# Kernel tuning notes

Measured on AMD Instinct MI355X. Metric: run time of the kernel, lower is better.

## Reference

```python
import jax, jax.numpy as jnp
import numpy as np

T, B, H = 1024, 4096, 4  # time steps, students, BKT params (l,f,g,s)


def setup_inputs() -> dict:
    key = jax.random.key(0)
    ks = jax.random.split(key, 6)
    # binary correctness sequences, like the original BKT data
    x = (jax.random.uniform(ks[0], (T, B, 1)) < 0.5).astype(jnp.float32)
    y = (jax.random.uniform(ks[1], (T, B, 1)) < 0.5).astype(jnp.float32)
    s = 1.0 / np.sqrt(H)  # torch nn.RNN default init: U(-1/sqrt(H), 1/sqrt(H))
    W_ih = jax.random.uniform(ks[2], (H, 1), minval=-s, maxval=s, dtype=jnp.float32)
    W_hh = jax.random.uniform(ks[3], (H, H), minval=-s, maxval=s, dtype=jnp.float32)
    b_ih = jax.random.uniform(ks[4], (H,), minval=-s, maxval=s, dtype=jnp.float32)
    b_hh = jax.random.uniform(ks[5], (H,), minval=-s, maxval=s, dtype=jnp.float32)
    prior = jnp.array([0.1], dtype=jnp.float32)
    return {"x": x, "y": y, "prior": prior, "W_ih": W_ih, "W_hh": W_hh,
            "b_ih": b_ih, "b_hh": b_hh}


def _bce(p, y):
    # torch BCELoss clamps log terms at -100
    logp = jnp.maximum(jnp.log(p), -100.0)
    log1mp = jnp.maximum(jnp.log(1.0 - p), -100.0)
    return -(y * logp + (1.0 - y) * log1mp).mean()


def _forward(x, y, prior, W_ih, W_hh, b_ih, b_hh):
    Bn = x.shape[1]
    Hn = W_hh.shape[0]

    # --- Elman RNN (tanh), seq-first, h0 = 0 ---
    def rnn_step(h, x_t):  # x_t: [B,1], h: [B,H]
        h = jnp.tanh(x_t @ W_ih.T + b_ih + h @ W_hh.T + b_hh)
        return h, h

    h0 = jnp.zeros((Bn, Hn), dtype=x.dtype)
    _, output = jax.lax.scan(rnn_step, h0, x)  # [T,B,H]
    params = (output + 1.0) / 2.0  # map tanh output into (0,1)

    # --- sequential nonlinear BKT latent recurrence ---
    latent0 = jnp.broadcast_to(jax.nn.sigmoid(prior), (Bn, 1)).astype(x.dtype)

    def bkt_step(latent, inp):
        p_t, y_t = inp  # p_t: [B,H], y_t: [B,1]
        l, f, g, s = p_t[:, 0:1], p_t[:, 1:2], p_t[:, 2:3], p_t[:, 3:4]
        correct = latent * (1 - s) + (1 - latent) * g
        k_t1 = latent * (1 - s) / (latent * (1 - s) + (1 - latent) * g)
        k_t0 = latent * s / (latent * s + (1 - latent) * (1 - g))
        m_t = k_t1 * correct + k_t0 * (1 - correct)
        next_latent = m_t * (1 - f) + (1 - m_t) * l
        return next_latent, (correct, next_latent, _bce(correct, y_t))

    _, (corrects, latents, losses) = jax.lax.scan(bkt_step, latent0, (params, y))
    loss = losses.mean()  # sum of per-step BCE / T
    return corrects, latents, loss


def reference(x, y, prior, W_ih, W_hh, b_ih, b_hh):
    return _forward(x, y, prior, W_ih, W_hh, b_ih, b_hh)
```

## Files before the change

### kernel.cpp

```cpp
#include <hip/hip_runtime.h>

#define TT 1024
#define BB 4096
#define CHUNK 64
#define WH 64
#define NCH (TT / CHUNK)
#define NB  (NCH * BB)

#define WS_A   1024
#define WS_B   (WS_A + NB)
#define WS_H   (WS_B + NB)
#define WS_XW  (WS_H + 4 * NB)

typedef float v2f __attribute__((ext_vector_type(2)));

struct StepC {
    v2f base01, base23, sw01, sw23;
    v2f c0_01, c0_23, c1_01, c1_23, c2_01, c2_23, c3_01, c3_23;
};

__device__ __forceinline__ StepC make_consts(const float* W_ih, const float* W_hh,
                                             const float* b_ih, const float* b_hh) {
    const float S = 2.8853900817779268f;
    float basev[4], swv[4], vv[4][4];
    #pragma unroll
    for (int jj = 0; jj < 4; ++jj) {
        float rowsum = W_hh[jj*4+0] + W_hh[jj*4+1] + W_hh[jj*4+2] + W_hh[jj*4+3];
        basev[jj] = S * (b_ih[jj] + b_hh[jj] + rowsum);
        swv[jj]   = S * W_ih[jj];
        #pragma unroll
        for (int kk = 0; kk < 4; ++kk) vv[jj][kk] = -2.f * S * W_hh[jj*4+kk];
    }
    StepC K;
    K.base01 = {basev[0], basev[1]}; K.base23 = {basev[2], basev[3]};
    K.sw01   = {swv[0],   swv[1]};   K.sw23   = {swv[2],   swv[3]};
    K.c0_01 = {vv[0][0], vv[1][0]};  K.c0_23 = {vv[2][0], vv[3][0]};
    K.c1_01 = {vv[0][1], vv[1][1]};  K.c1_23 = {vv[2][1], vv[3][1]};
    K.c2_01 = {vv[0][2], vv[1][2]};  K.c2_23 = {vv[2][2], vv[3][2]};
    K.c3_01 = {vv[0][3], vv[1][3]};  K.c3_23 = {vv[2][3], vv[3][3]};
    return K;
}

__device__ __forceinline__ void rnn_step(const StepC& K, float xf,
                                         float& r0, float& r1, float& r2, float& r3) {
    v2f xv  = {xf, xf};
    v2f r0b = {r0, r0}, r1b = {r1, r1}, r2b = {r2, r2}, r3b = {r3, r3};
    v2f z01 = __builtin_elementwise_fma(xv, K.sw01, K.base01);
    v2f z23 = __builtin_elementwise_fma(xv, K.sw23, K.base23);
    z01 = __builtin_elementwise_fma(r0b, K.c0_01, z01);
    z23 = __builtin_elementwise_fma(r0b, K.c0_23, z23);
    z01 = __builtin_elementwise_fma(r1b, K.c1_01, z01);
    z23 = __builtin_elementwise_fma(r1b, K.c1_23, z23);
    z01 = __builtin_elementwise_fma(r2b, K.c2_01, z01);
    z23 = __builtin_elementwise_fma(r2b, K.c2_23, z23);
    z01 = __builtin_elementwise_fma(r3b, K.c3_01, z01);
    z23 = __builtin_elementwise_fma(r3b, K.c3_23, z23);
    r0 = __builtin_amdgcn_rcpf(__builtin_amdgcn_exp2f(z01.x) + 1.0f);
    r1 = __builtin_amdgcn_rcpf(__builtin_amdgcn_exp2f(z01.y) + 1.0f);
    r2 = __builtin_amdgcn_rcpf(__builtin_amdgcn_exp2f(z23.x) + 1.0f);
    r3 = __builtin_amdgcn_rcpf(__builtin_amdgcn_exp2f(z23.y) + 1.0f);
}

__launch_bounds__(64, 1)
__global__ void bkt_pass1(const float* __restrict__ x,
                          const float* __restrict__ W_ih, const float* __restrict__ W_hh,
                          const float* __restrict__ b_ih, const float* __restrict__ b_hh,
                          float* __restrict__ ws)
{
    const int lane = threadIdx.x;
    const int c  = blockIdx.x >> 6;
    const int eg = blockIdx.x & 63;
    const int e  = eg * 64 + lane;
    const int t0 = c * CHUNK;
    const int t_start = (c == 0) ? 0 : (t0 - WH);
    const float* xp = x + (size_t)t_start * BB + e;

    float bufA[32], bufB[32];
    auto issueA = [&](int wd) {
        const float* p = xp + (size_t)wd * 32 * BB;
        #pragma unroll
        for (int i = 0; i < 32; ++i) bufA[i] = p[(size_t)i * BB];
    };
    auto issueB = [&](int wd) {
        const float* p = xp + (size_t)wd * 32 * BB;
        #pragma unroll
        for (int i = 0; i < 32; ++i) bufB[i] = p[(size_t)i * BB];
    };
    auto packA = [&]() -> unsigned {
        unsigned m = 0;
        #pragma unroll
        for (int i = 0; i < 32; ++i) if (bufA[i] != 0.0f) m |= (1u << i);
        return m;
    };
    auto packB = [&]() -> unsigned {
        unsigned m = 0;
        #pragma unroll
        for (int i = 0; i < 32; ++i) if (bufB[i] != 0.0f) m |= (1u << i);
        return m;
    };

    const StepC K = make_consts(W_ih, W_hh, b_ih, b_hh);
    float r0 = 0.5f, r1 = 0.5f, r2 = 0.5f, r3 = 0.5f;

    auto run32_warm = [&](unsigned m) {
        #pragma unroll 8
        for (int i = 0; i < 32; ++i)
            rnn_step(K, (float)((m >> i) & 1u), r0, r1, r2, r3);
    };

    float A = 1.0f, Bacc = 0.0f;
    auto run32_acc = [&](unsigned m) {
        #pragma unroll 8
        for (int i = 0; i < 32; ++i) {
            rnn_step(K, (float)((m >> i) & 1u), r0, r1, r2, r3);
            float a = (r0 + r1) - 1.0f;
            Bacc = fmaf(a, Bacc, 1.0f - r0);
            A *= a;
        }
    };

    float s0, s1, s2, s3;
    unsigned mo0, mo1;

    if (c == 0) {
        issueA(0); issueB(1);
        s0 = s1 = s2 = s3 = 0.5f;
        mo0 = packA();
        run32_acc(mo0);
        mo1 = packB();
        run32_acc(mo1);
    } else {
        issueA(0); issueB(1);
        unsigned mw0 = packA();
        issueA(2);
        run32_warm(mw0);
        unsigned mw1 = packB();
        issueB(3);
        run32_warm(mw1);
        s0 = r0; s1 = r1; s2 = r2; s3 = r3;
        mo0 = packA();
        run32_acc(mo0);
        mo1 = packB();
        run32_acc(mo1);
    }

    const int idx = c * BB + e;
    ws[WS_A + idx] = A;
    ws[WS_B + idx] = Bacc;
    ws[WS_H + 0 * NB + idx] = s0;
    ws[WS_H + 1 * NB + idx] = s1;
    ws[WS_H + 2 * NB + idx] = s2;
    ws[WS_H + 3 * NB + idx] = s3;
    unsigned* wsu = (unsigned*)ws;
    wsu[WS_XW + 0 * NB + idx] = mo0;
    wsu[WS_XW + 1 * NB + idx] = mo1;
}

__launch_bounds__(64, 1)
__global__ void bkt_pass2(const float* __restrict__ y, const float* __restrict__ prior,
                          const float* __restrict__ W_ih, const float* __restrict__ W_hh,
                          const float* __restrict__ b_ih, const float* __restrict__ b_hh,
                          float* __restrict__ out, float* __restrict__ ws)
{
    const int lane = threadIdx.x;
    const int c  = blockIdx.x >> 6;
    const int eg = blockIdx.x & 63;
    const int e  = eg * 64 + lane;
    const int t0 = c * CHUNK;
    const int idx = c * BB + e;

    float Av[NCH - 1], Bv[NCH - 1];
    #pragma unroll
    for (int cc = 0; cc < NCH - 1; ++cc) {
        Av[cc] = ws[WS_A + cc * BB + e];
        Bv[cc] = ws[WS_B + cc * BB + e];
    }
    float r0 = ws[WS_H + 0 * NB + idx];
    float r1 = ws[WS_H + 1 * NB + idx];
    float r2 = ws[WS_H + 2 * NB + idx];
    float r3 = ws[WS_H + 3 * NB + idx];
    const unsigned* wsu = (const unsigned*)ws;
    unsigned mo0 = wsu[WS_XW + 0 * NB + idx];
    unsigned mo1 = wsu[WS_XW + 1 * NB + idx];

    const float* ypb = y + (size_t)t0 * BB + e;
    float yA[32], yB[32];
    #pragma unroll
    for (int i = 0; i < 32; ++i) yA[i] = ypb[(size_t)i * BB];
    #pragma unroll
    for (int i = 0; i < 32; ++i) yB[i] = ypb[(size_t)(i + 32) * BB];

    const StepC K = make_consts(W_ih, W_hh, b_ih, b_hh);

    float lat = 1.0f / (1.0f + __builtin_amdgcn_exp2f(-1.4426950408889634f * prior[0]));
    #pragma unroll
    for (int cc = 0; cc < NCH - 1; ++cc)
        lat = (cc < c) ? fmaf(Av[cc], lat, Bv[cc]) : lat;

    unsigned yw0 = 0, yw1 = 0;
    #pragma unroll
    for (int i = 0; i < 32; ++i) {
        if (yA[i] != 0.0f) yw0 |= (1u << i);
        if (yB[i] != 0.0f) yw1 |= (1u << i);
    }

    float* cO = out + (size_t)t0 * BB + e;
    float* lO = cO + (size_t)TT * BB;
    float lossAcc = 0.0f;

    auto outblock = [&](unsigned mw, unsigned yw, int tb) {
        float prod = 1.0f;
        #pragma unroll 8
        for (int i = 0; i < 32; ++i) {
            rnn_step(K, (float)((mw >> i) & 1u), r0, r1, r2, r3);
            float corr = fmaf(lat, (r2 + r3) - 1.0f, 1.0f - r2);
            float nl   = fmaf(lat, (r0 + r1) - 1.0f, 1.0f - r0);
            const size_t off = (size_t)(tb + i) * BB;
            cO[off] = corr;
            lO[off] = nl;
            float lp = ((yw >> i) & 1u) ? corr : (1.0f - corr);
            prod *= lp;
            if ((i & 7) == 7) {
                lossAcc += __builtin_amdgcn_logf(prod) * 0.6931471805599453f;
                prod = 1.0f;
            }
            lat = nl;
        }
    };
    outblock(mo0, yw0, 0);
    outblock(mo1, yw1, 32);

    #pragma unroll
    for (int o = 32; o >= 1; o >>= 1) lossAcc += __shfl_xor(lossAcc, o, 64);
    if (lane == 0) ws[blockIdx.x] = lossAcc;
}

__global__ void reduce_k(const float* __restrict__ part, float* __restrict__ loss) {
    float acc = 0.f;
    for (int i = threadIdx.x; i < 1024; i += 256) acc += part[i];
    #pragma unroll
    for (int o = 32; o >= 1; o >>= 1) acc += __shfl_xor(acc, o, 64);
    __shared__ float w[4];
    if ((threadIdx.x & 63) == 0) w[threadIdx.x >> 6] = acc;
    __syncthreads();
    if (threadIdx.x == 0) {
        float t = w[0] + w[1] + w[2] + w[3];
        *loss = t * (-1.0f / ((float)TT * (float)BB));
    }
}

extern "C" void kernel_launch(void* const* d_in, const int* in_sizes, int n_in,
                              void* d_out, int out_size, void* d_ws, size_t ws_size,
                              hipStream_t stream) {
    const float* x    = (const float*)d_in[0];
    const float* y    = (const float*)d_in[1];
    const float* pr   = (const float*)d_in[2];
    const float* W_ih = (const float*)d_in[3];
    const float* W_hh = (const float*)d_in[4];
    const float* b_ih = (const float*)d_in[5];
    const float* b_hh = (const float*)d_in[6];
    float* out = (float*)d_out;
    float* ws  = (float*)d_ws;

    bkt_pass1<<<NCH * 64, 64, 0, stream>>>(x, W_ih, W_hh, b_ih, b_hh, ws);
    bkt_pass2<<<NCH * 64, 64, 0, stream>>>(y, pr, W_ih, W_hh, b_ih, b_hh, out, ws);
    reduce_k<<<1, 256, 0, stream>>>(ws, out + 2 * (size_t)TT * BB);
}
```

Before: 115.7 us.

## Fuse both BKT passes and loss reduction into one cooperative kernel with grid sync

Merges the two passes into a single cooperative kernel. The RNN hidden state and x bitmasks stay in registers across a grid-wide sync, so they are no longer written to and reread from workspace. The y loads are issued during the accumulation phase to overlap with compute. The separate reduce kernel is replaced by an atomic loss accumulation, with the last-arriving block writing the final loss. This removes two launches and workspace round-trips, but adds grid-sync cost, requires all 1024 blocks to be co-resident, and makes the loss sum order nondeterministic.

```diff
diff --git a/kernel.cpp b/kernel.cpp
--- a/kernel.cpp
+++ b/kernel.cpp
@@ -1,4 +1,7 @@
 #include <hip/hip_runtime.h>
+#include <hip/hip_cooperative_groups.h>
+
+namespace cg = cooperative_groups;
 
 #define TT 1024
 #define BB 4096
@@ -7,10 +10,10 @@
 #define NCH (TT / CHUNK)
 #define NB  (NCH * BB)
 
-#define WS_A   1024
-#define WS_B   (WS_A + NB)
-#define WS_H   (WS_B + NB)
-#define WS_XW  (WS_H + 4 * NB)
+#define WS_LOSS 0
+#define WS_CNT  1
+#define WS_A    64
+#define WS_B    (WS_A + NB)
 
 typedef float v2f __attribute__((ext_vector_type(2)));
 
@@ -62,102 +65,8 @@
 }
 
 __launch_bounds__(64, 1)
-__global__ void bkt_pass1(const float* __restrict__ x,
-                          const float* __restrict__ W_ih, const float* __restrict__ W_hh,
-                          const float* __restrict__ b_ih, const float* __restrict__ b_hh,
-                          float* __restrict__ ws)
-{
-    const int lane = threadIdx.x;
-    const int c  = blockIdx.x >> 6;
-    const int eg = blockIdx.x & 63;
-    const int e  = eg * 64 + lane;
-    const int t0 = c * CHUNK;
-    const int t_start = (c == 0) ? 0 : (t0 - WH);
-    const float* xp = x + (size_t)t_start * BB + e;
-
-    float bufA[32], bufB[32];
-    auto issueA = [&](int wd) {
-        const float* p = xp + (size_t)wd * 32 * BB;
-        #pragma unroll
-        for (int i = 0; i < 32; ++i) bufA[i] = p[(size_t)i * BB];
-    };
-    auto issueB = [&](int wd) {
-        const float* p = xp + (size_t)wd * 32 * BB;
-        #pragma unroll
-        for (int i = 0; i < 32; ++i) bufB[i] = p[(size_t)i * BB];
-    };
-    auto packA = [&]() -> unsigned {
-        unsigned m = 0;
-        #pragma unroll
-        for (int i = 0; i < 32; ++i) if (bufA[i] != 0.0f) m |= (1u << i);
-        return m;
-    };
-    auto packB = [&]() -> unsigned {
-        unsigned m = 0;
-        #pragma unroll
-        for (int i = 0; i < 32; ++i) if (bufB[i] != 0.0f) m |= (1u << i);
-        return m;
-    };
-
-    const StepC K = make_consts(W_ih, W_hh, b_ih, b_hh);
-    float r0 = 0.5f, r1 = 0.5f, r2 = 0.5f, r3 = 0.5f;
-
-    auto run32_warm = [&](unsigned m) {
-        #pragma unroll 8
-        for (int i = 0; i < 32; ++i)
-            rnn_step(K, (float)((m >> i) & 1u), r0, r1, r2, r3);
-    };
-
-    float A = 1.0f, Bacc = 0.0f;
-    auto run32_acc = [&](unsigned m) {
-        #pragma unroll 8
-        for (int i = 0; i < 32; ++i) {
-            rnn_step(K, (float)((m >> i) & 1u), r0, r1, r2, r3);
-            float a = (r0 + r1) - 1.0f;
-            Bacc = fmaf(a, Bacc, 1.0f - r0);
-            A *= a;
-        }
-    };
-
-    float s0, s1, s2, s3;
-    unsigned mo0, mo1;
-
-    if (c == 0) {
-        issueA(0); issueB(1);
-        s0 = s1 = s2 = s3 = 0.5f;
-        mo0 = packA();
-        run32_acc(mo0);
-        mo1 = packB();
-        run32_acc(mo1);
-    } else {
-        issueA(0); issueB(1);
-        unsigned mw0 = packA();
-        issueA(2);
-        run32_warm(mw0);
-        unsigned mw1 = packB();
-        issueB(3);
-        run32_warm(mw1);
-        s0 = r0; s1 = r1; s2 = r2; s3 = r3;
-        mo0 = packA();
-        run32_acc(mo0);
-        mo1 = packB();
-        run32_acc(mo1);
-    }
-
-    const int idx = c * BB + e;
-    ws[WS_A + idx] = A;
-    ws[WS_B + idx] = Bacc;
-    ws[WS_H + 0 * NB + idx] = s0;
-    ws[WS_H + 1 * NB + idx] = s1;
-    ws[WS_H + 2 * NB + idx] = s2;
-    ws[WS_H + 3 * NB + idx] = s3;
-    unsigned* wsu = (unsigned*)ws;
-    wsu[WS_XW + 0 * NB + idx] = mo0;
-    wsu[WS_XW + 1 * NB + idx] = mo1;
-}
-
-__launch_bounds__(64, 1)
-__global__ void bkt_pass2(const float* __restrict__ y, const float* __restrict__ prior,
+__global__ void bkt_fused(const float* __restrict__ x, const float* __restrict__ y,
+                          const float* __restrict__ prior,
                           const float* __restrict__ W_ih, const float* __restrict__ W_hh,
                           const float* __restrict__ b_ih, const float* __restrict__ b_hh,
                           float* __restrict__ out, float* __restrict__ ws)
@@ -167,7 +76,94 @@
     const int eg = blockIdx.x & 63;
     const int e  = eg * 64 + lane;
     const int t0 = c * CHUNK;
+    const int t_start = (c == 0) ? 0 : (t0 - WH);
+    const float* xp  = x + (size_t)t_start * BB + e;
+    const float* ypb = y + (size_t)t0 * BB + e;
+
+    if (blockIdx.x == 0 && lane == 0) {
+        ws[WS_LOSS] = 0.0f;
+        ((unsigned*)ws)[WS_CNT] = 0u;
+    }
+
+    float bufA[32], bufB[32];
+    auto issueA = [&](const float* p) {
+        #pragma unroll
+        for (int i = 0; i < 32; ++i) bufA[i] = p[(size_t)i * BB];
+    };
+    auto issueB = [&](const float* p) {
+        #pragma unroll
+        for (int i = 0; i < 32; ++i) bufB[i] = p[(size_t)i * BB];
+    };
+    auto packA = [&]() -> unsigned {
+        unsigned m = 0;
+        #pragma unroll
+        for (int i = 0; i < 32; ++i) if (bufA[i] != 0.0f) m |= (1u << i);
+        return m;
+    };
+    auto packB = [&]() -> unsigned {
+        unsigned m = 0;
+        #pragma unroll
+        for (int i = 0; i < 32; ++i) if (bufB[i] != 0.0f) m |= (1u << i);
+        return m;
+    };
+
+    issueA(xp); issueB(xp + (size_t)32 * BB);
+    const float pr0 = prior[0];
+    const StepC K = make_consts(W_ih, W_hh, b_ih, b_hh);
+
+    float r0 = 0.5f, r1 = 0.5f, r2 = 0.5f, r3 = 0.5f;
+    float A = 1.0f, Bacc = 0.0f;
+
+    auto run32_warm = [&](unsigned m) {
+        #pragma unroll 8
+        for (int i = 0; i < 32; ++i)
+            rnn_step(K, (float)((m >> i) & 1u), r0, r1, r2, r3);
+    };
+    auto run32_acc = [&](unsigned m) {
+        #pragma unroll 8
+        for (int i = 0; i < 32; ++i) {
+            rnn_step(K, (float)((m >> i) & 1u), r0, r1, r2, r3);
+            float a = (r0 + r1) - 1.0f;
+            Bacc = fmaf(a, Bacc, 1.0f - r0);
+            A *= a;
+        }
+    };
+
+    float s0, s1, s2, s3;
+    unsigned mo0, mo1, yw0, yw1;
+
+    if (c == 0) {
+        s0 = s1 = s2 = s3 = 0.5f;
+        mo0 = packA();
+        issueA(ypb);
+        run32_acc(mo0);
+        mo1 = packB();
+        issueB(ypb + (size_t)32 * BB);
+        run32_acc(mo1);
+        yw0 = packA(); yw1 = packB();
+    } else {
+        unsigned mw0 = packA();
+        issueA(xp + (size_t)64 * BB);
+        run32_warm(mw0);
+        unsigned mw1 = packB();
+        issueB(xp + (size_t)96 * BB);
+        run32_warm(mw1);
+        s0 = r0; s1 = r1; s2 = r2; s3 = r3;
+        mo0 = packA();
+        issueA(ypb);
+        run32_acc(mo0);
+        mo1 = packB();
+        issueB(ypb + (size_t)32 * BB);
+        run32_acc(mo1);
+        yw0 = packA(); yw1 = packB();
+    }
+
     const int idx = c * BB + e;
+    ws[WS_A + idx] = A;
+    ws[WS_B + idx] = Bacc;
+
+    __threadfence();
+    cg::this_grid().sync();
 
     float Av[NCH - 1], Bv[NCH - 1];
     #pragma unroll
@@ -175,35 +171,12 @@
         Av[cc] = ws[WS_A + cc * BB + e];
         Bv[cc] = ws[WS_B + cc * BB + e];
     }
-    float r0 = ws[WS_H + 0 * NB + idx];
-    float r1 = ws[WS_H + 1 * NB + idx];
-    float r2 = ws[WS_H + 2 * NB + idx];
-    float r3 = ws[WS_H + 3 * NB + idx];
-    const unsigned* wsu = (const unsigned*)ws;
-    unsigned mo0 = wsu[WS_XW + 0 * NB + idx];
-    unsigned mo1 = wsu[WS_XW + 1 * NB + idx];
-
-    const float* ypb = y + (size_t)t0 * BB + e;
-    float yA[32], yB[32];
-    #pragma unroll
-    for (int i = 0; i < 32; ++i) yA[i] = ypb[(size_t)i * BB];
-    #pragma unroll
-    for (int i = 0; i < 32; ++i) yB[i] = ypb[(size_t)(i + 32) * BB];
-
-    const StepC K = make_consts(W_ih, W_hh, b_ih, b_hh);
-
-    float lat = 1.0f / (1.0f + __builtin_amdgcn_exp2f(-1.4426950408889634f * prior[0]));
+    float lat = 1.0f / (1.0f + __builtin_amdgcn_exp2f(-1.4426950408889634f * pr0));
     #pragma unroll
     for (int cc = 0; cc < NCH - 1; ++cc)
         lat = (cc < c) ? fmaf(Av[cc], lat, Bv[cc]) : lat;
 
-    unsigned yw0 = 0, yw1 = 0;
-    #pragma unroll
-    for (int i = 0; i < 32; ++i) {
-        if (yA[i] != 0.0f) yw0 |= (1u << i);
-        if (yB[i] != 0.0f) yw1 |= (1u << i);
-    }
-
+    r0 = s0; r1 = s1; r2 = s2; r3 = s3;
     float* cO = out + (size_t)t0 * BB + e;
     float* lO = cO + (size_t)TT * BB;
     float lossAcc = 0.0f;
@@ -232,20 +205,15 @@
 
     #pragma unroll
     for (int o = 32; o >= 1; o >>= 1) lossAcc += __shfl_xor(lossAcc, o, 64);
-    if (lane == 0) ws[blockIdx.x] = lossAcc;
-}
-
-__global__ void reduce_k(const float* __restrict__ part, float* __restrict__ loss) {
-    float acc = 0.f;
-    for (int i = threadIdx.x; i < 1024; i += 256) acc += part[i];
-    #pragma unroll
-    for (int o = 32; o >= 1; o >>= 1) acc += __shfl_xor(acc, o, 64);
-    __shared__ float w[4];
-    if ((threadIdx.x & 63) == 0) w[threadIdx.x >> 6] = acc;
-    __syncthreads();
-    if (threadIdx.x == 0) {
-        float t = w[0] + w[1] + w[2] + w[3];
-        *loss = t * (-1.0f / ((float)TT * (float)BB));
+
+    if (lane == 0) {
+        atomicAdd(&ws[WS_LOSS], lossAcc);
+        __threadfence();
+        unsigned t = atomicAdd(&((unsigned*)ws)[WS_CNT], 1u);
+        if (t == (unsigned)(NCH * 64 - 1)) {
+            float tot = atomicAdd(&ws[WS_LOSS], 0.0f);
+            out[2 * (size_t)TT * BB] = tot * (-1.0f / ((float)TT * (float)BB));
+        }
     }
 }
 
@@ -262,7 +230,8 @@
     float* out = (float*)d_out;
     float* ws  = (float*)d_ws;
 
-    bkt_pass1<<<NCH * 64, 64, 0, stream>>>(x, W_ih, W_hh, b_ih, b_hh, ws);
-    bkt_pass2<<<NCH * 64, 64, 0, stream>>>(y, pr, W_ih, W_hh, b_ih, b_hh, out, ws);
-    reduce_k<<<1, 256, 0, stream>>>(ws, out + 2 * (size_t)TT * BB);
-}
+    void* args[] = {(void*)&x, (void*)&y, (void*)&pr, (void*)&W_ih, (void*)&W_hh,
+                    (void*)&b_ih, (void*)&b_hh, (void*)&out, (void*)&ws};
+    hipLaunchCooperativeKernel((void*)bkt_fused, dim3(NCH * 64), dim3(64),
+                               args, 0, stream);
+}
```

After: 217.9 us. 1.88x slower.
